# Kernel tuning notes

Measured on AMD Instinct MI355X. Metric: run time of the kernel, lower is better.

## Reference

```python
import jax, jax.numpy as jnp
import numpy as np

THRESHOLD = 0.1  # matches init kwarg 'threshold'


def setup_inputs() -> dict:
    key = jax.random.key(0)
    ks = jax.random.split(key, 4)
    B, T, D = 16, 4096, 1024   # batch, tokens(=patch_h*patch_w), d_model
    E, R = 8, 64               # experts, lora rank
    inputs = jax.random.normal(ks[0], (B, T, D), dtype=jnp.float32)
    gate_w = jax.random.normal(ks[1], (D, E), dtype=jnp.float32) * (1.0 / np.sqrt(D))
    gate_b = jnp.zeros((E,), dtype=jnp.float32)
    lora_A = jax.random.normal(ks[2], (E, D, R), dtype=jnp.float32) * (1.0 / np.sqrt(D))
    lora_B = jax.random.normal(ks[3], (E, R, D), dtype=jnp.float32) * (1.0 / np.sqrt(R))
    return {"inputs": inputs, "gate_w": gate_w, "gate_b": gate_b,
            "lora_A": lora_A, "lora_B": lora_B, "patch_h": 64, "patch_w": 64}


def reference(inputs, gate_w, gate_b, lora_A, lora_B, patch_h, patch_w):
    # patch_h / patch_w are unused by 'linear' LoRA experts (kept for signature parity)
    D = inputs.shape[-1]
    x = inputs.reshape(-1, D)                                  # [N, D]
    gate_logits = jax.nn.softmax(x @ gate_w + gate_b, axis=-1)  # [N, E]
    selected = (gate_logits >= THRESHOLD).astype(x.dtype)       # threshold gate
    weights = gate_logits * selected
    wsum = jnp.sum(weights, axis=-1, keepdims=True)
    wsum = jnp.where(wsum == 0, jnp.ones_like(wsum), wsum)
    weights = weights / wsum                                    # renormalized weights [N, E]
    # Dense equivalent of per-expert gather/scatter: tokens with weight 0 contribute nothing,
    # identical to the boolean-indexed accumulation in the torch code.
    h = jnp.einsum('nd,edr->ner', x, lora_A)                    # [N, E, R]
    out = jnp.einsum('ner,erd,ne->nd', h, lora_B, weights)      # weighted combine [N, D]
    return out.reshape(inputs.shape[:-1] + (D,))
```

## Files before the change

kernel.cpp:

```cpp
#include <hip/hip_runtime.h>
#include <stdint.h>
#include <stddef.h>


typedef float f32x4 __attribute__((ext_vector_type(4)));
typedef short bf16x8 __attribute__((ext_vector_type(8)));

#define MFMA_16x16x32(A, B, C) __builtin_amdgcn_mfma_f32_16x16x32_bf16((A), (B), (C), 0, 0, 0)
#define SCHED_FENCE() __builtin_amdgcn_sched_barrier(0)
#define BAR() __builtin_amdgcn_s_barrier()
#define WAIT_LGKM0() asm volatile("s_waitcnt lgkmcnt(0)" ::: "memory")
#define WAIT_VM0_LGKM0() asm volatile("s_waitcnt vmcnt(0) lgkmcnt(0)" ::: "memory")

__device__ __forceinline__ unsigned short f2bf(float f) {
    union { float f; unsigned int u; } v;
    v.f = f;
    unsigned int u = v.u;
    u += 0x7FFFu + ((u >> 16) & 1u);
    return (unsigned short)(u >> 16);
}

__device__ __forceinline__ void load16_lds(unsigned short* lds, const unsigned short* g) {
    __builtin_amdgcn_global_load_lds(
        (const __attribute__((address_space(1))) unsigned int*)g,
        (__attribute__((address_space(3))) unsigned int*)lds, 16, 0, 0);
}

__global__ __launch_bounds__(256) void convert_pack(
        const float* __restrict__ LA, const float* __restrict__ LB,
        unsigned short* __restrict__ A_P, unsigned short* __restrict__ B_P) {
    int gid = blockIdx.x * 256 + threadIdx.x;
    if (gid < 524288) {
        int j = gid & 7, l = (gid >> 3) & 63, cblk = (gid >> 9) & 31, kblk = gid >> 14;
        int d = kblk * 32 + (l >> 4) * 8 + j;
        int col = cblk * 16 + (l & 15);
        int e = col >> 6, r = col & 63;
        A_P[gid] = f2bf(LA[((size_t)e * 1024 + d) * 64 + r]);
    } else {
        int idx = gid - 524288;
        int j = idx & 7, l = (idx >> 3) & 63, cblk = (idx >> 9) & 63, kblk = idx >> 15;
        int k = kblk * 32 + (l >> 4) * 8 + j;
        int d = cblk * 16 + (l & 15);
        int e = k >> 6, r = k & 63;
        B_P[idx] = f2bf(LB[((size_t)e * 64 + r) * 1024 + d]);
    }
}

__global__ __launch_bounds__(256) void gate_kernel(
        const float* __restrict__ X, const float* __restrict__ GW,
        const float* __restrict__ GB, float* __restrict__ Wg) {
    __shared__ float gwt[8 * 1024];
    int tid = threadIdx.x;

    {
        float r[4][8];
#pragma unroll
        for (int j = 0; j < 4; ++j) {
            const f32x4* gp = (const f32x4*)(GW + (size_t)(tid * 4 + j) * 8);
            f32x4 g0 = gp[0], g1 = gp[1];
#pragma unroll
            for (int q = 0; q < 4; ++q) { r[j][q] = g0[q]; r[j][4 + q] = g1[q]; }
        }
#pragma unroll
        for (int e = 0; e < 8; ++e) {
            f32x4 v;
#pragma unroll
            for (int j = 0; j < 4; ++j) v[j] = r[j][e];
            *(f32x4*)&gwt[e * 1024 + tid * 4] = v;
        }
    }
    __syncthreads();

    int row = blockIdx.x * 16 + (tid >> 4);
    int sub = tid & 15;
    const float* xr = X + (size_t)row * 1024 + sub * 4;

    f32x4 xs[16];
#pragma unroll
    for (int it = 0; it < 16; ++it) xs[it] = *(const f32x4*)(xr + it * 64);

    float lg[8];
#pragma unroll
    for (int e = 0; e < 8; ++e) lg[e] = 0.f;

#pragma unroll
    for (int it = 0; it < 16; ++it) {
        f32x4 g[8];
#pragma unroll
        for (int e = 0; e < 8; ++e)
            g[e] = *(const f32x4*)&gwt[e * 1024 + it * 64 + sub * 4];
        f32x4 x = xs[it];
#pragma unroll
        for (int e = 0; e < 8; ++e) {
            lg[e] += x[0] * g[e][0];
            lg[e] += x[1] * g[e][1];
            lg[e] += x[2] * g[e][2];
            lg[e] += x[3] * g[e][3];
        }
    }
#pragma unroll
    for (int s = 1; s < 16; s <<= 1) {
#pragma unroll
        for (int e = 0; e < 8; ++e) lg[e] += __shfl_xor(lg[e], s, 16);
    }
    float p[8], m = -1e30f, ssum = 0.f;
#pragma unroll
    for (int e = 0; e < 8; ++e) { lg[e] += GB[e]; m = fmaxf(m, lg[e]); }
#pragma unroll
    for (int e = 0; e < 8; ++e) { p[e] = expf(lg[e] - m); ssum += p[e]; }
    float inv = 1.f / ssum;
    float wv[8], wsum = 0.f;
#pragma unroll
    for (int e = 0; e < 8; ++e) {
        float pe = p[e] * inv;
        wv[e] = (pe >= 0.1f) ? pe : 0.f;
        wsum += wv[e];
    }
    if (wsum == 0.f) wsum = 1.f;
    float invw = 1.f / wsum;
    if (sub < 8) Wg[(size_t)row * 8 + sub] = wv[sub] * invw;
}

__global__ __launch_bounds__(512, 4) void fused_kernel(
        const float* __restrict__ X, const unsigned short* __restrict__ A_P,
        const unsigned short* __restrict__ B_P, const float* __restrict__ Wg,
        float* __restrict__ Out) {
    __shared__ union SM1 {
        struct {
            unsigned short a[2][32 * 512];
            unsigned short x[2][64 * 40];
        } p;
        unsigned short hb[64 * 520];
    } sm;
    __shared__ float wl[512];

    int tid = threadIdx.x;
    int lane = tid & 63;
    int w = tid >> 6;
    int blk = blockIdx.x;
    int row = tid >> 3;
    int sub = tid & 7;

    wl[tid] = Wg[(size_t)blk * 512 + tid];

    const float* xp = X + (size_t)blk * 64 * 1024 + (size_t)row * 1024 + sub * 4;
    unsigned short* aCur = sm.p.a[0];
    unsigned short* aNxt = sm.p.a[1];
    unsigned short* xCur = sm.p.x[0];
    unsigned short* xNxt = sm.p.x[1];

    {
        const unsigned short* asrc = A_P + tid * 8;
#pragma unroll
        for (int i = 0; i < 4; ++i)
            load16_lds(&aCur[tid * 8 + i * 4096], asrc + i * 4096);
    }
    SCHED_FENCE();
    f32x4 xv0 = *(const f32x4*)(xp);
    f32x4 xv_hold = *(const f32x4*)(xp + 32);
    {
        unsigned int lo = (unsigned int)f2bf(xv0[0]) | ((unsigned int)f2bf(xv0[1]) << 16);
        unsigned int hi = (unsigned int)f2bf(xv0[2]) | ((unsigned int)f2bf(xv0[3]) << 16);
        *((uint2*)&xCur[row * 40 + sub * 4]) = make_uint2(lo, hi);
    }

    f32x4 acc[4][4] = {};
    for (int kb = 0; kb < 31; ++kb) {
        const unsigned short* asrc = A_P + (size_t)(kb + 1) * 16384 + tid * 8;
#pragma unroll
        for (int i = 0; i < 4; ++i)
            load16_lds(&aNxt[tid * 8 + i * 4096], asrc + i * 4096);
        SCHED_FENCE();
        int kbn = (kb + 2 <= 31) ? kb + 2 : 31;
        f32x4 xv_new = *(const f32x4*)(xp + (size_t)kbn * 32);
        unsigned int lo = (unsigned int)f2bf(xv_hold[0]) | ((unsigned int)f2bf(xv_hold[1]) << 16);
        unsigned int hi = (unsigned int)f2bf(xv_hold[2]) | ((unsigned int)f2bf(xv_hold[3]) << 16);
        *((uint2*)&xNxt[row * 40 + sub * 4]) = make_uint2(lo, hi);
        WAIT_LGKM0();
        SCHED_FENCE();
        BAR();
        SCHED_FENCE();
        bf16x8 af[4], bv[4];
#pragma unroll
        for (int m = 0; m < 4; ++m)
            af[m] = *(const bf16x8*)&xCur[(m * 16 + (lane & 15)) * 40 + (lane >> 4) * 8];
#pragma unroll
        for (int n = 0; n < 4; ++n)
            bv[n] = *(const bf16x8*)&aCur[(w * 4 + n) * 512 + lane * 8];
#pragma unroll
        for (int m = 0; m < 4; ++m)
#pragma unroll
            for (int n = 0; n < 4; ++n)
                acc[m][n] = MFMA_16x16x32(af[m], bv[n], acc[m][n]);
        BAR();
        unsigned short* t;
        t = aCur; aCur = aNxt; aNxt = t;
        t = xCur; xCur = xNxt; xNxt = t;
        xv_hold = xv_new;
    }
    WAIT_VM0_LGKM0();
    SCHED_FENCE();
    BAR();
    SCHED_FENCE();
    {
        bf16x8 af[4], bv[4];
#pragma unroll
        for (int m = 0; m < 4; ++m)
            af[m] = *(const bf16x8*)&xCur[(m * 16 + (lane & 15)) * 40 + (lane >> 4) * 8];
#pragma unroll
        for (int n = 0; n < 4; ++n)
            bv[n] = *(const bf16x8*)&aCur[(w * 4 + n) * 512 + lane * 8];
#pragma unroll
        for (int m = 0; m < 4; ++m)
#pragma unroll
            for (int n = 0; n < 4; ++n)
                acc[m][n] = MFMA_16x16x32(af[m], bv[n], acc[m][n]);
    }
    __syncthreads();

#pragma unroll
    for (int m = 0; m < 4; ++m) {
        float wv[4];
#pragma unroll
        for (int r = 0; r < 4; ++r)
            wv[r] = wl[(m * 16 + (lane >> 4) * 4 + r) * 8 + w];
#pragma unroll
        for (int n = 0; n < 4; ++n) {
            int col = w * 64 + n * 16 + (lane & 15);
#pragma unroll
            for (int r = 0; r < 4; ++r) {
                int rr = m * 16 + (lane >> 4) * 4 + r;
                sm.hb[rr * 520 + col] = f2bf(acc[m][n][r] * wv[r]);
            }
        }
    }
    __syncthreads();

#pragma unroll
    for (int h = 0; h < 2; ++h) {
        f32x4 acc2[4][4] = {};
        int cb0 = w * 8 + h * 4;
        for (int kc = 0; kc < 16; ++kc) {
            bf16x8 af2[4], bv2[4];
#pragma unroll
            for (int n = 0; n < 4; ++n)
                bv2[n] = *(const bf16x8*)(B_P + (((size_t)kc * 64 + cb0 + n) * 64 + lane) * 8);
#pragma unroll
            for (int m = 0; m < 4; ++m)
                af2[m] = *(const bf16x8*)&sm.hb[(m * 16 + (lane & 15)) * 520 + kc * 32 + (lane >> 4) * 8];
#pragma unroll
            for (int m = 0; m < 4; ++m)
#pragma unroll
                for (int n = 0; n < 4; ++n)
                    acc2[m][n] = MFMA_16x16x32(af2[m], bv2[n], acc2[m][n]);
        }
        size_t rb = (size_t)blk * 64;
        int cb = w * 128 + h * 64;
#pragma unroll
        for (int m = 0; m < 4; ++m)
#pragma unroll
            for (int n = 0; n < 4; ++n) {
                int col = cb + n * 16 + (lane & 15);
#pragma unroll
                for (int r = 0; r < 4; ++r) {
                    size_t rrow = rb + m * 16 + (lane >> 4) * 4 + r;
                    Out[rrow * 1024 + col] = acc2[m][n][r];
                }
            }
    }
}

extern "C" void kernel_launch(void* const* d_in, const int* in_sizes, int n_in,
                              void* d_out, int out_size, void* d_ws, size_t ws_size,
                              hipStream_t stream) {
    const float* X  = (const float*)d_in[0];
    const float* GW = (const float*)d_in[1];
    const float* GB = (const float*)d_in[2];
    const float* LA = (const float*)d_in[3];
    const float* LB = (const float*)d_in[4];
    float* Out = (float*)d_out;

    char* ws = (char*)d_ws;
    float*          Wg  = (float*)ws;
    unsigned short* A_P = (unsigned short*)(ws + (2u << 20));
    unsigned short* B_P = (unsigned short*)(ws + (3u << 20));

    convert_pack<<<4096, 256, 0, stream>>>(LA, LB, A_P, B_P);
    gate_kernel<<<4096, 256, 0, stream>>>(X, GW, GB, Wg);
    fused_kernel<<<1024, 512, 0, stream>>>(X, A_P, B_P, Wg, Out);
}
```

Before: 310.2 us.

## Swizzle X tile into MFMA fragment layout and prefetch B fragments

Changes the shared-memory layout of the bf16 X tile so each lane's MFMA A-fragment is contiguous (m*512 + lane*8), replacing the padded row-major layout. This removes strided LDS reads and shrinks the buffer. The second GEMM now software-pipelines the global loads of B_P fragments one k-step ahead, so load latency overlaps the MFMAs at the cost of extra registers. The output store loop is also reordered by row, with columns innermost.

Result: slower. 323.3 us (+4.2%).

```diff
diff --git a/kernel.cpp b/kernel.cpp
--- a/kernel.cpp
+++ b/kernel.cpp
@@ -128,7 +128,7 @@
     __shared__ union SM1 {
         struct {
             unsigned short a[2][32 * 512];
-            unsigned short x[2][64 * 40];
+            unsigned short x[2][2048];
         } p;
         unsigned short hb[64 * 520];
     } sm;
@@ -144,6 +144,8 @@
     wl[tid] = Wg[(size_t)blk * 512 + tid];
 
     const float* xp = X + (size_t)blk * 64 * 1024 + (size_t)row * 1024 + sub * 4;
+    int xw_off = (row >> 4) * 512 + (((row & 15) | ((sub >> 1) << 4)) * 8) + (sub & 1) * 4;
+
     unsigned short* aCur = sm.p.a[0];
     unsigned short* aNxt = sm.p.a[1];
     unsigned short* xCur = sm.p.x[0];
@@ -161,7 +163,7 @@
     {
         unsigned int lo = (unsigned int)f2bf(xv0[0]) | ((unsigned int)f2bf(xv0[1]) << 16);
         unsigned int hi = (unsigned int)f2bf(xv0[2]) | ((unsigned int)f2bf(xv0[3]) << 16);
-        *((uint2*)&xCur[row * 40 + sub * 4]) = make_uint2(lo, hi);
+        *((uint2*)&xCur[xw_off]) = make_uint2(lo, hi);
     }
 
     f32x4 acc[4][4] = {};
@@ -175,7 +177,7 @@
         f32x4 xv_new = *(const f32x4*)(xp + (size_t)kbn * 32);
         unsigned int lo = (unsigned int)f2bf(xv_hold[0]) | ((unsigned int)f2bf(xv_hold[1]) << 16);
         unsigned int hi = (unsigned int)f2bf(xv_hold[2]) | ((unsigned int)f2bf(xv_hold[3]) << 16);
-        *((uint2*)&xNxt[row * 40 + sub * 4]) = make_uint2(lo, hi);
+        *((uint2*)&xNxt[xw_off]) = make_uint2(lo, hi);
         WAIT_LGKM0();
         SCHED_FENCE();
         BAR();
@@ -183,7 +185,7 @@
         bf16x8 af[4], bv[4];
 #pragma unroll
         for (int m = 0; m < 4; ++m)
-            af[m] = *(const bf16x8*)&xCur[(m * 16 + (lane & 15)) * 40 + (lane >> 4) * 8];
+            af[m] = *(const bf16x8*)&xCur[m * 512 + lane * 8];
 #pragma unroll
         for (int n = 0; n < 4; ++n)
             bv[n] = *(const bf16x8*)&aCur[(w * 4 + n) * 512 + lane * 8];
@@ -206,7 +208,7 @@
         bf16x8 af[4], bv[4];
 #pragma unroll
         for (int m = 0; m < 4; ++m)
-            af[m] = *(const bf16x8*)&xCur[(m * 16 + (lane & 15)) * 40 + (lane >> 4) * 8];
+            af[m] = *(const bf16x8*)&xCur[m * 512 + lane * 8];
 #pragma unroll
         for (int n = 0; n < 4; ++n)
             bv[n] = *(const bf16x8*)&aCur[(w * 4 + n) * 512 + lane * 8];
@@ -240,32 +242,41 @@
     for (int h = 0; h < 2; ++h) {
         f32x4 acc2[4][4] = {};
         int cb0 = w * 8 + h * 4;
+        bf16x8 bvC[4], bvN[4];
+#pragma unroll
+        for (int n = 0; n < 4; ++n)
+            bvC[n] = *(const bf16x8*)(B_P + (((size_t)cb0 + n) * 64 + lane) * 8);
         for (int kc = 0; kc < 16; ++kc) {
-            bf16x8 af2[4], bv2[4];
-#pragma unroll
-            for (int n = 0; n < 4; ++n)
-                bv2[n] = *(const bf16x8*)(B_P + (((size_t)kc * 64 + cb0 + n) * 64 + lane) * 8);
+            bf16x8 af2[4];
 #pragma unroll
             for (int m = 0; m < 4; ++m)
                 af2[m] = *(const bf16x8*)&sm.hb[(m * 16 + (lane & 15)) * 520 + kc * 32 + (lane >> 4) * 8];
+            if (kc < 15) {
+#pragma unroll
+                for (int n = 0; n < 4; ++n)
+                    bvN[n] = *(const bf16x8*)(B_P + (((size_t)(kc + 1) * 64 + cb0 + n) * 64 + lane) * 8);
+            }
 #pragma unroll
             for (int m = 0; m < 4; ++m)
 #pragma unroll
                 for (int n = 0; n < 4; ++n)
-                    acc2[m][n] = MFMA_16x16x32(af2[m], bv2[n], acc2[m][n]);
+                    acc2[m][n] = MFMA_16x16x32(af2[m], bvC[n], acc2[m][n]);
+            if (kc < 15) {
+#pragma unroll
+                for (int n = 0; n < 4; ++n) bvC[n] = bvN[n];
+            }
         }
         size_t rb = (size_t)blk * 64;
         int cb = w * 128 + h * 64;
 #pragma unroll
         for (int m = 0; m < 4; ++m)
 #pragma unroll
-            for (int n = 0; n < 4; ++n) {
-                int col = cb + n * 16 + (lane & 15);
-#pragma unroll
-                for (int r = 0; r < 4; ++r) {
-                    size_t rrow = rb + m * 16 + (lane >> 4) * 4 + r;
-                    Out[rrow * 1024 + col] = acc2[m][n][r];
-                }
+            for (int r = 0; r < 4; ++r) {
+                size_t rrow = rb + m * 16 + (lane >> 4) * 4 + r;
+                float* orow = Out + rrow * 1024 + cb + (lane & 15);
+#pragma unroll
+                for (int n = 0; n < 4; ++n)
+                    orow[n * 16] = acc2[m][n][r];
             }
     }
 }
```
